# Optimization experiments

Measured on AMD Instinct MI355X. Metric: run time of the kernel, lower is better.

## Reference

```python
import jax, jax.numpy as jnp
import numpy as np


def conv2d(x, w, pad, groups=1):
    # x: [B,Cin,H,W], w: [Cout,Cin/groups,K,K]
    return jax.lax.conv_general_dilated(
        x, w, (1, 1), [(pad, pad), (pad, pad)],
        dimension_numbers=('NCHW', 'OIHW', 'NCHW'),
        feature_group_count=groups)


def setup_inputs() -> dict:
    key = jax.random.key(0)
    ks = jax.random.split(key, 24)
    B, C, H, W = 16, 512, 32, 128          # batch, encoder_dim, feature map
    Da, Ds, De, Dm = 512, 256, 256, 1024   # att_dim, state_dim, embed_dim, mem_dim
    V, Dmerge = 1000, 512
    K, P = 11, 5
    Din = De + C + Dm                       # GRU input dim = 1792
    s = 0.02
    rn = lambda k, shp, sc=1.0: jax.random.normal(k, shp, jnp.float32) * sc
    return {
        'encode': rn(ks[0], (B, C, H, W)),
        'encode_pro': rn(ks[1], (B, Da, H, W)),
        'encode_mask': jnp.ones((B, 1, H, W), jnp.float32),
        'state': rn(ks[2], (B, Ds)),
        'pre_weight': jax.random.uniform(ks[3], (B, 1, H, W), jnp.float32),
        'cum_weight': jax.random.uniform(ks[4], (B, 1, H, W), jnp.float32),
        'context': rn(ks[5], (B, C)),
        'cond_mem': rn(ks[6], (B, Dm)),
        'cond_weight': jax.random.uniform(ks[7], (B, 2, H, W), jnp.float32),
        'label_id': jax.random.randint(ks[8], (B,), 0, V),
        # ImageAttention params (all bias-free per source)
        'w_wt': rn(ks[9], (Da, 1, K, K), s),
        'w_cwt': rn(ks[10], (Da, 1, K, K), s),
        'w_condwt': rn(ks[11], (2 * Da, 1, K, K), s),   # groups=2
        'w_energy': rn(ks[12], (Da,), s),               # 1x1 conv -> vector
        'w_state': rn(ks[13], (Da, Ds), s),
        'w_ctx': rn(ks[14], (Da, C), s),
        'w_cond': rn(ks[15], (Da, Dm), s),
        # GRU params
        'w_i2s': rn(ks[16], (Ds, Din), s), 'b_i2s': jnp.zeros((Ds,), jnp.float32),
        'w_i2g': rn(ks[17], (2 * Ds, Din), s), 'b_i2g': jnp.zeros((2 * Ds,), jnp.float32),
        'w_s2g': rn(ks[18], (2 * Ds, Ds), s),
        'w_h2h': rn(ks[19], (Ds, Ds), s),
        # Readout params
        'embed_table': rn(ks[20], (V, De), s),
        'w_l1': rn(ks[21], (Dmerge, De + Ds + C), s), 'b_l1': jnp.zeros((Dmerge,), jnp.float32),
        'w_l2': rn(ks[22], (V, Dmerge), s), 'b_l2': jnp.zeros((V,), jnp.float32),
    }


def reference(encode, encode_pro, encode_mask, state, pre_weight, cum_weight,
              context, cond_mem, cond_weight, label_id, w_wt, w_cwt, w_condwt,
              w_energy, w_state, w_ctx, w_cond, w_i2s, b_i2s, w_i2g, b_i2g,
              w_s2g, w_h2h, embed_table, w_l1, b_l1, w_l2, b_l2):
    P = (w_wt.shape[-1] - 1) // 2
    Da = w_energy.shape[0]
    B, C, H, W = encode.shape
    # --- ImageAttention ---
    t_pre = conv2d(pre_weight, w_wt, P)           # [B,Da,H,W]
    t_cum = conv2d(cum_weight, w_cwt, P)          # [B,Da,H,W]
    t_cw = conv2d(cond_weight, w_condwt, P, groups=2)
    t_cw = t_cw.reshape(B, 2, Da, H, W).sum(1)    # [B,Da,H,W]
    st = state @ w_state.T + context @ w_ctx.T + cond_mem @ w_cond.T  # [B,Da]
    concat_info = jnp.tanh(st[:, :, None, None] + t_pre + t_cum + t_cw + encode_pro)
    energies = jnp.einsum('bchw,c->bhw', concat_info, w_energy)
    energies = energies + (encode_mask[:, 0] - 1.0) * 1e8
    att = jax.nn.softmax(energies.reshape(B, H * W), axis=1)
    new_weight = att.reshape(B, 1, H, W)
    new_cum_weight = cum_weight + new_weight
    ctx = jnp.einsum('bchw,bhw->bc', encode, new_weight[:, 0])  # [B,C]
    # --- GRU transition (data = [embed, ctx, cond_mem]) ---
    embed = embed_table[label_id]
    data = jnp.concatenate([embed, ctx, cond_mem], axis=1)
    gate = data @ w_i2g.T + b_i2g + state @ w_s2g.T
    Ds = state.shape[1]
    update_g = jax.nn.sigmoid(gate[:, :Ds])
    reset_g = jax.nn.sigmoid(gate[:, Ds:])
    state_hat = jnp.tanh(data @ w_i2s.T + b_i2s + (state * reset_g) @ w_h2h.T)
    new_state = update_g * state_hat + (1.0 - update_g) * state
    # --- Readout.step ---
    merged = jnp.concatenate([embed, new_state, ctx], axis=1)
    hid = jax.nn.relu(merged @ w_l1.T + b_l1)
    readout = hid @ w_l2.T + b_l2                  # [B,V]
    return readout
```

## Files before the change

### kernel.cpp

```cpp
#include <hip/hip_runtime.h>
#include <math.h>

typedef unsigned short u16;
typedef __bf16 bf16x8 __attribute__((ext_vector_type(8)));
typedef float f32x4 __attribute__((ext_vector_type(4)));

__device__ u16   g_A_pack[16 * 512 * 32];
__device__ float g_st[16 * 512];
__device__ float g_epart[2 * 16 * 4096];
__device__ float g_energ[16 * 4096];
__device__ float g_data[16 * 1792];
__device__ float g_merged[16 * 1024];
__device__ float g_update[16 * 256];
__device__ float g_reset[16 * 256];
__device__ float g_i2s[16 * 256];
__device__ float g_hid[16 * 512];

__device__ __forceinline__ u16 f2bf(float f) {
    unsigned u = __float_as_uint(f);
    u = (u + 0x7FFFu + ((u >> 16) & 1u)) >> 16;
    return (u16)u;
}
__device__ __forceinline__ float fast_tanh(float x) {
    return 1.0f - 2.0f / (__expf(2.0f * x) + 1.0f);
}
__device__ __forceinline__ float sigmoidf_(float x) {
    return 1.0f / (1.0f + __expf(-x));
}

__global__ void k_prep(const float* __restrict__ w_wt, const float* __restrict__ w_cwt,
                       const float* __restrict__ w_condwt) {
    int idx = blockIdx.x * blockDim.x + threadIdx.x;
    if (idx >= 512 * 512) return;
    int d = idx >> 9, k = idx & 511;
    float f = 0.f;
    if (k < 484) {
        int c = k / 121, rem = k % 121;
        if (c == 0)      f = w_wt[d * 121 + rem];
        else if (c == 1) f = w_cwt[d * 121 + rem];
        else if (c == 2) f = w_condwt[d * 121 + rem];
        else             f = w_condwt[(512 + d) * 121 + rem];
    }
    int ks = k >> 5, kl = k & 31;
    g_A_pack[(ks * 512 + d) * 32 + kl] = f2bf(f);
}

__global__ void k_st(const float* __restrict__ state, const float* __restrict__ context,
                     const float* __restrict__ cond_mem, const float* __restrict__ w_state,
                     const float* __restrict__ w_ctx, const float* __restrict__ w_cond) {
    int wid = (blockIdx.x * blockDim.x + threadIdx.x) >> 6;
    int lane = threadIdx.x & 63;
    if (wid >= 16 * 512) return;
    int b = wid >> 9, d = wid & 511;
    float acc = 0.f;
    for (int k = lane; k < 256; k += 64)  acc += state[b * 256 + k]    * w_state[d * 256 + k];
    for (int k = lane; k < 512; k += 64)  acc += context[b * 512 + k]  * w_ctx[d * 512 + k];
    for (int k = lane; k < 1024; k += 64) acc += cond_mem[b * 1024 + k] * w_cond[d * 1024 + k];
    for (int off = 32; off; off >>= 1) acc += __shfl_down(acc, off, 64);
    if (lane == 0) g_st[b * 512 + d] = acc;
}

__global__ void k_e0(const int* __restrict__ label, const float* __restrict__ embed_table,
                     const float* __restrict__ cond_mem) {
    int b = blockIdx.x, tid = threadIdx.x;
    int lbl = label[b];
    if (tid < 256) {
        float ev = embed_table[lbl * 256 + tid];
        g_data[b * 1792 + tid] = ev;
        g_merged[b * 1024 + tid] = ev;
    }
    for (int k = tid; k < 1024; k += 256)
        g_data[b * 1792 + 768 + k] = cond_mem[b * 1024 + k];
}

__global__ __launch_bounds__(256, 3) void k_conv_energy(
    const float* __restrict__ pre_w, const float* __restrict__ cum_w, const float* __restrict__ cond_w,
    const float* __restrict__ encode_pro, const float* __restrict__ w_energy)
{
    __shared__ __align__(16) u16 src[4][11][80];
    __shared__ __align__(16) u16 bchunk[2][64][40];
    __shared__ float ered[4][64];

    const int blk = blockIdx.x;
    const int quad = blk & 3;
    const int h = (blk >> 2) & 31;
    const int b = blk >> 7;
    const int dbase = (quad >> 1) * 256;
    const int px0 = (quad & 1) * 64;

    const int tid = threadIdx.x;
    const int lane = tid & 63, wv = tid >> 6;
    const int lr = lane & 15, lg = lane >> 4;

    for (int t = tid; t < 4 * 11 * 80; t += 256) {
        int c = t / (11 * 80);
        int rem = t % (11 * 80);
        int i = rem / 80, x = rem % 80;
        int row = h + i - 5, w = px0 - 5 + x;
        u16 v = 0;
        if (x < 74 && row >= 0 && row < 32 && w >= 0 && w < 128) {
            const float* img = (c == 0) ? pre_w + b * 4096
                             : (c == 1) ? cum_w + b * 4096
                             : (c == 2) ? cond_w + b * 8192
                                        : cond_w + b * 8192 + 4096;
            v = f2bf(img[row * 128 + w]);
        }
        src[c][i][x] = v;
    }
    __syncthreads();

    const int kl = tid & 31;
    const int n0 = tid >> 5;
#define BUILD(KS, BUF)                                                        \
    {                                                                         \
        int kg = (KS) * 32 + kl;                                              \
        int c = 0, i = 0, jj = 0;                                             \
        bool ok = (kg < 484);                                                 \
        if (ok) { c = kg / 121; int r2 = kg % 121; i = r2 / 11; jj = r2 % 11; } \
        _Pragma("unroll")                                                     \
        for (int rep = 0; rep < 8; ++rep) {                                   \
            int n = n0 + rep * 8;                                             \
            bchunk[BUF][n][kl] = ok ? src[c][i][n + jj] : (u16)0;             \
        }                                                                     \
    }

    f32x4 acc[4][4];
#pragma unroll
    for (int mt = 0; mt < 4; ++mt)
#pragma unroll
        for (int nt = 0; nt < 4; ++nt) {
            f32x4 z = {0.f, 0.f, 0.f, 0.f};
            acc[mt][nt] = z;
        }

    BUILD(0, 0);
    __syncthreads();

    for (int ks = 0; ks < 16; ++ks) {
        const int cur = ks & 1;
        bf16x8 afr[4];
#pragma unroll
        for (int mt = 0; mt < 4; ++mt) {
            int d = dbase + wv * 64 + mt * 16 + lr;
            afr[mt] = *reinterpret_cast<const bf16x8*>(&g_A_pack[(ks * 512 + d) * 32 + lg * 8]);
        }
        bf16x8 bfr[4];
#pragma unroll
        for (int nt = 0; nt < 4; ++nt)
            bfr[nt] = *reinterpret_cast<const bf16x8*>(&bchunk[cur][nt * 16 + lr][lg * 8]);

        if (ks < 15) BUILD(ks + 1, cur ^ 1);

#pragma unroll
        for (int mt = 0; mt < 4; ++mt)
#pragma unroll
            for (int nt = 0; nt < 4; ++nt)
                acc[mt][nt] = __builtin_amdgcn_mfma_f32_16x16x32_bf16(afr[mt], bfr[nt], acc[mt][nt], 0, 0, 0);
        __syncthreads();
    }
#undef BUILD

    float e[4] = {0.f, 0.f, 0.f, 0.f};
#pragma unroll
    for (int mt = 0; mt < 4; ++mt) {
#pragma unroll
        for (int r = 0; r < 4; ++r) {
            int d = dbase + wv * 64 + mt * 16 + lg * 4 + r;
            float stv = g_st[b * 512 + d];
            float wev = w_energy[d];
            const float* ep_row = encode_pro + ((size_t)(b * 512 + d) * 32 + h) * 128 + px0;
#pragma unroll
            for (int nt = 0; nt < 4; ++nt) {
                float val = stv + acc[mt][nt][r] + ep_row[nt * 16 + lr];
                e[nt] += wev * fast_tanh(val);
            }
        }
    }
#pragma unroll
    for (int nt = 0; nt < 4; ++nt) {
        float v = e[nt];
        v += __shfl_xor(v, 16, 64);
        v += __shfl_xor(v, 32, 64);
        if (lane < 16) ered[wv][nt * 16 + lane] = v;
    }
    __syncthreads();
    if (tid < 64) {
        float v = ered[0][tid] + ered[1][tid] + ered[2][tid] + ered[3][tid];
        g_epart[(size_t)(quad >> 1) * 65536 + b * 4096 + h * 128 + px0 + tid] = v;
    }
}

__global__ void k_softmax(const float* __restrict__ encode_mask) {
    __shared__ float red[256];
    int b = blockIdx.x, tid = threadIdx.x;
    float v[16];
    float mx = -1e30f;
#pragma unroll
    for (int i = 0; i < 16; ++i) {
        int idx = b * 4096 + tid + i * 256;
        float ev = g_epart[idx] + g_epart[65536 + idx] + (encode_mask[idx] - 1.0f) * 1e8f;
        v[i] = ev; mx = fmaxf(mx, ev);
    }
    red[tid] = mx; __syncthreads();
    for (int s = 128; s; s >>= 1) { if (tid < s) red[tid] = fmaxf(red[tid], red[tid + s]); __syncthreads(); }
    mx = red[0]; __syncthreads();
    float sum = 0.f;
#pragma unroll
    for (int i = 0; i < 16; ++i) { v[i] = __expf(v[i] - mx); sum += v[i]; }
    red[tid] = sum; __syncthreads();
    for (int s = 128; s; s >>= 1) { if (tid < s) red[tid] += red[tid + s]; __syncthreads(); }
    float inv = 1.0f / red[0];
#pragma unroll
    for (int i = 0; i < 16; ++i) g_energ[b * 4096 + tid + i * 256] = v[i] * inv;
}

__global__ void k_ctx(const float* __restrict__ encode) {
    int wid = (blockIdx.x * blockDim.x + threadIdx.x) >> 6;
    int lane = threadIdx.x & 63;
    if (wid >= 16 * 512) return;
    int b = wid >> 9, c = wid & 511;
    const float* e = encode + (size_t)wid * 4096;
    const float* a = g_energ + b * 4096;
    float acc = 0.f;
#pragma unroll
    for (int it = 0; it < 16; ++it) {
        int base = it * 256 + lane * 4;
        float4 ev = *reinterpret_cast<const float4*>(&e[base]);
        float4 av = *reinterpret_cast<const float4*>(&a[base]);
        acc += ev.x * av.x + ev.y * av.y + ev.z * av.z + ev.w * av.w;
    }
    for (int off = 32; off; off >>= 1) acc += __shfl_down(acc, off, 64);
    if (lane == 0) { g_data[b * 1792 + 256 + c] = acc; g_merged[b * 1024 + 512 + c] = acc; }
}

__global__ void k_e1(const float* __restrict__ state,
                     const float* __restrict__ w_i2g, const float* __restrict__ b_i2g,
                     const float* __restrict__ w_s2g, const float* __restrict__ w_i2s,
                     const float* __restrict__ b_i2s) {
    int wid = (blockIdx.x * blockDim.x + threadIdx.x) >> 6;
    int lane = threadIdx.x & 63;
    if (wid >= 16 * 768) return;
    int b = wid / 768, o = wid % 768;
    const float* dt = g_data + b * 1792;
    float acc = 0.f;
    if (o < 512) {
        const float* wr = w_i2g + o * 1792;
        for (int k = lane; k < 1792; k += 64) acc += dt[k] * wr[k];
        const float* wsg = w_s2g + o * 256;
        for (int k = lane; k < 256; k += 64) acc += state[b * 256 + k] * wsg[k];
    } else {
        const float* wr = w_i2s + (o - 512) * 1792;
        for (int k = lane; k < 1792; k += 64) acc += dt[k] * wr[k];
    }
    for (int off = 32; off; off >>= 1) acc += __shfl_down(acc, off, 64);
    if (lane == 0) {
        if (o < 256)       g_update[b * 256 + o]        = sigmoidf_(acc + b_i2g[o]);
        else if (o < 512)  g_reset[b * 256 + (o - 256)] = sigmoidf_(acc + b_i2g[o]);
        else               g_i2s[b * 256 + (o - 512)]   = acc + b_i2s[o - 512];
    }
}

__global__ void k_e2(const float* __restrict__ state, const float* __restrict__ w_h2h) {
    int wid = (blockIdx.x * blockDim.x + threadIdx.x) >> 6;
    int lane = threadIdx.x & 63;
    if (wid >= 16 * 256) return;
    int b = wid >> 8, d = wid & 255;
    const float* wr = w_h2h + d * 256;
    float acc = 0.f;
    for (int k = lane; k < 256; k += 64)
        acc += state[b * 256 + k] * g_reset[b * 256 + k] * wr[k];
    for (int off = 32; off; off >>= 1) acc += __shfl_down(acc, off, 64);
    if (lane == 0) {
        float sh = fast_tanh(g_i2s[b * 256 + d] + acc);
        float u = g_update[b * 256 + d];
        g_merged[b * 1024 + 256 + d] = u * sh + (1.f - u) * state[b * 256 + d];
    }
}

__global__ void k_e3(const float* __restrict__ w_l1, const float* __restrict__ b_l1) {
    int wid = (blockIdx.x * blockDim.x + threadIdx.x) >> 6;
    int lane = threadIdx.x & 63;
    if (wid >= 16 * 512) return;
    int b = wid >> 9, m = wid & 511;
    const float* mg = g_merged + b * 1024;
    const float* wr = w_l1 + m * 1024;
    float acc = 0.f;
    for (int k = lane; k < 1024; k += 64) acc += mg[k] * wr[k];
    for (int off = 32; off; off >>= 1) acc += __shfl_down(acc, off, 64);
    if (lane == 0) g_hid[b * 512 + m] = fmaxf(acc + b_l1[m], 0.f);
}

__global__ void k_e4(const float* __restrict__ w_l2, const float* __restrict__ b_l2,
                     float* __restrict__ out) {
    int wid = (blockIdx.x * blockDim.x + threadIdx.x) >> 6;
    int lane = threadIdx.x & 63;
    if (wid >= 16 * 1000) return;
    int b = wid / 1000, v = wid % 1000;
    const float* hd = g_hid + b * 512;
    const float* wr = w_l2 + v * 512;
    float acc = 0.f;
    for (int k = lane; k < 512; k += 64) acc += hd[k] * wr[k];
    for (int off = 32; off; off >>= 1) acc += __shfl_down(acc, off, 64);
    if (lane == 0) out[b * 1000 + v] = acc + b_l2[v];
}

extern "C" void kernel_launch(void* const* d_in, const int* in_sizes, int n_in,
                              void* d_out, int out_size, void* d_ws, size_t ws_size,
                              hipStream_t stream) {
    static const int EXP[28] = {
        33554432, 33554432, 65536, 4096, 65536, 65536, 8192, 16384, 131072, 16,
        61952, 61952, 123904, 512, 131072, 262144, 524288, 458752, 256, 917504,
        512, 131072, 65536, 256000, 524288, 512, 512000, 1000};
    if (n_in != 28) return;
    for (int i = 0; i < 28; ++i)
        if (in_sizes[i] != EXP[i]) return;

    const float* encode      = (const float*)d_in[0];
    const float* encode_pro  = (const float*)d_in[1];
    const float* encode_mask = (const float*)d_in[2];
    const float* state       = (const float*)d_in[3];
    const float* pre_weight  = (const float*)d_in[4];
    const float* cum_weight  = (const float*)d_in[5];
    const float* context     = (const float*)d_in[6];
    const float* cond_mem    = (const float*)d_in[7];
    const float* cond_weight = (const float*)d_in[8];
    const int*   label_id    = (const int*)d_in[9];
    const float* w_wt     = (const float*)d_in[10];
    const float* w_cwt    = (const float*)d_in[11];
    const float* w_condwt = (const float*)d_in[12];
    const float* w_energy = (const float*)d_in[13];
    const float* w_state  = (const float*)d_in[14];
    const float* w_ctx    = (const float*)d_in[15];
    const float* w_cond   = (const float*)d_in[16];
    const float* w_i2s    = (const float*)d_in[17];
    const float* b_i2s    = (const float*)d_in[18];
    const float* w_i2g    = (const float*)d_in[19];
    const float* b_i2g    = (const float*)d_in[20];
    const float* w_s2g    = (const float*)d_in[21];
    const float* w_h2h    = (const float*)d_in[22];
    const float* embed_t  = (const float*)d_in[23];
    const float* w_l1     = (const float*)d_in[24];
    const float* b_l1     = (const float*)d_in[25];
    const float* w_l2     = (const float*)d_in[26];
    const float* b_l2     = (const float*)d_in[27];
    float* out = (float*)d_out;
    (void)d_ws; (void)ws_size;

    k_prep<<<1024, 256, 0, stream>>>(w_wt, w_cwt, w_condwt);
    k_st<<<2048, 256, 0, stream>>>(state, context, cond_mem, w_state, w_ctx, w_cond);
    k_e0<<<16, 256, 0, stream>>>(label_id, embed_t, cond_mem);
    k_conv_energy<<<2048, 256, 0, stream>>>(pre_weight, cum_weight, cond_weight,
                                            encode_pro, w_energy);
    k_softmax<<<16, 256, 0, stream>>>(encode_mask);
    k_ctx<<<2048, 256, 0, stream>>>(encode);
    k_e1<<<3072, 256, 0, stream>>>(state, w_i2g, b_i2g, w_s2g, w_i2s, b_i2s);
    k_e2<<<1024, 256, 0, stream>>>(state, w_h2h);
    k_e3<<<2048, 256, 0, stream>>>(w_l1, b_l1);
    k_e4<<<4000, 256, 0, stream>>>(w_l2, b_l2, out);
}
```

Before: 188.4 us.

## Build full im2col tile once per block and cover all channels per block

The conv-energy kernel now uses 512-thread blocks that each cover all 512 attention channels for a 64-pixel half-row, instead of splitting channels across two blocks. The im2col B tile for every K chunk is built once into a 64x520 shared buffer before the MFMA loop. This removes the per-step rebuild and barrier, halves the duplicated source staging and im2col work, and drops the two-partial energy sum in softmax. In exchange it uses more shared memory per block, leaves threads beyond 484 filling zero padding, and may lower occupancy.

```diff
diff --git a/kernel.cpp b/kernel.cpp
--- a/kernel.cpp
+++ b/kernel.cpp
@@ -7,7 +7,7 @@
 
 __device__ u16   g_A_pack[16 * 512 * 32];
 __device__ float g_st[16 * 512];
-__device__ float g_epart[2 * 16 * 4096];
+__device__ float g_eraw[16 * 4096];
 __device__ float g_energ[16 * 4096];
 __device__ float g_data[16 * 1792];
 __device__ float g_merged[16 * 1024];
@@ -73,26 +73,25 @@
         g_data[b * 1792 + 768 + k] = cond_mem[b * 1024 + k];
 }
 
-__global__ __launch_bounds__(256, 3) void k_conv_energy(
+__global__ __launch_bounds__(512, 2) void k_conv_energy(
     const float* __restrict__ pre_w, const float* __restrict__ cum_w, const float* __restrict__ cond_w,
     const float* __restrict__ encode_pro, const float* __restrict__ w_energy)
 {
     __shared__ __align__(16) u16 src[4][11][80];
-    __shared__ __align__(16) u16 bchunk[2][64][40];
-    __shared__ float ered[4][64];
+    __shared__ __align__(16) u16 bchunk[64][520];
+    __shared__ float ered[8][64];
 
     const int blk = blockIdx.x;
-    const int quad = blk & 3;
-    const int h = (blk >> 2) & 31;
-    const int b = blk >> 7;
-    const int dbase = (quad >> 1) * 256;
-    const int px0 = (quad & 1) * 64;
+    const int pxh = blk & 1;
+    const int h = (blk >> 1) & 31;
+    const int b = blk >> 6;
+    const int px0 = pxh * 64;
 
     const int tid = threadIdx.x;
     const int lane = tid & 63, wv = tid >> 6;
     const int lr = lane & 15, lg = lane >> 4;
 
-    for (int t = tid; t < 4 * 11 * 80; t += 256) {
+    for (int t = tid; t < 4 * 11 * 80; t += 512) {
         int c = t / (11 * 80);
         int rem = t % (11 * 80);
         int i = rem / 80, x = rem % 80;
@@ -109,20 +108,20 @@
     }
     __syncthreads();
 
-    const int kl = tid & 31;
-    const int n0 = tid >> 5;
-#define BUILD(KS, BUF)                                                        \
-    {                                                                         \
-        int kg = (KS) * 32 + kl;                                              \
-        int c = 0, i = 0, jj = 0;                                             \
-        bool ok = (kg < 484);                                                 \
-        if (ok) { c = kg / 121; int r2 = kg % 121; i = r2 / 11; jj = r2 % 11; } \
-        _Pragma("unroll")                                                     \
-        for (int rep = 0; rep < 8; ++rep) {                                   \
-            int n = n0 + rep * 8;                                             \
-            bchunk[BUF][n][kl] = ok ? src[c][i][n + jj] : (u16)0;             \
-        }                                                                     \
-    }
+    {
+        const int k = tid;
+        if (k < 484) {
+            int c = k / 121, rem = k % 121;
+            int i = rem / 11, jj = rem % 11;
+            const u16* s = &src[c][i][jj];
+#pragma unroll 8
+            for (int n = 0; n < 64; ++n) bchunk[n][k] = s[n];
+        } else {
+#pragma unroll 8
+            for (int n = 0; n < 64; ++n) bchunk[n][k] = 0;
+        }
+    }
+    __syncthreads();
 
     f32x4 acc[4][4];
 #pragma unroll
@@ -133,39 +132,32 @@
             acc[mt][nt] = z;
         }
 
-    BUILD(0, 0);
-    __syncthreads();
-
+#pragma unroll 2
     for (int ks = 0; ks < 16; ++ks) {
-        const int cur = ks & 1;
         bf16x8 afr[4];
 #pragma unroll
         for (int mt = 0; mt < 4; ++mt) {
-            int d = dbase + wv * 64 + mt * 16 + lr;
+            int d = wv * 64 + mt * 16 + lr;
             afr[mt] = *reinterpret_cast<const bf16x8*>(&g_A_pack[(ks * 512 + d) * 32 + lg * 8]);
         }
         bf16x8 bfr[4];
 #pragma unroll
         for (int nt = 0; nt < 4; ++nt)
-            bfr[nt] = *reinterpret_cast<const bf16x8*>(&bchunk[cur][nt * 16 + lr][lg * 8]);
-
-        if (ks < 15) BUILD(ks + 1, cur ^ 1);
+            bfr[nt] = *reinterpret_cast<const bf16x8*>(&bchunk[nt * 16 + lr][ks * 32 + lg * 8]);
 
 #pragma unroll
         for (int mt = 0; mt < 4; ++mt)
 #pragma unroll
             for (int nt = 0; nt < 4; ++nt)
                 acc[mt][nt] = __builtin_amdgcn_mfma_f32_16x16x32_bf16(afr[mt], bfr[nt], acc[mt][nt], 0, 0, 0);
-        __syncthreads();
-    }
-#undef BUILD
+    }
 
     float e[4] = {0.f, 0.f, 0.f, 0.f};
 #pragma unroll
     for (int mt = 0; mt < 4; ++mt) {
 #pragma unroll
         for (int r = 0; r < 4; ++r) {
-            int d = dbase + wv * 64 + mt * 16 + lg * 4 + r;
+            int d = wv * 64 + mt * 16 + lg * 4 + r;
             float stv = g_st[b * 512 + d];
             float wev = w_energy[d];
             const float* ep_row = encode_pro + ((size_t)(b * 512 + d) * 32 + h) * 128 + px0;
@@ -185,8 +177,10 @@
     }
     __syncthreads();
     if (tid < 64) {
-        float v = ered[0][tid] + ered[1][tid] + ered[2][tid] + ered[3][tid];
-        g_epart[(size_t)(quad >> 1) * 65536 + b * 4096 + h * 128 + px0 + tid] = v;
+        float v = 0.f;
+#pragma unroll
+        for (int w = 0; w < 8; ++w) v += ered[w][tid];
+        g_eraw[b * 4096 + h * 128 + px0 + tid] = v;
     }
 }
 
@@ -198,7 +192,7 @@
 #pragma unroll
     for (int i = 0; i < 16; ++i) {
         int idx = b * 4096 + tid + i * 256;
-        float ev = g_epart[idx] + g_epart[65536 + idx] + (encode_mask[idx] - 1.0f) * 1e8f;
+        float ev = g_eraw[idx] + (encode_mask[idx] - 1.0f) * 1e8f;
         v[i] = ev; mx = fmaxf(mx, ev);
     }
     red[tid] = mx; __syncthreads();
@@ -349,7 +343,7 @@
     k_prep<<<1024, 256, 0, stream>>>(w_wt, w_cwt, w_condwt);
     k_st<<<2048, 256, 0, stream>>>(state, context, cond_mem, w_state, w_ctx, w_cond);
     k_e0<<<16, 256, 0, stream>>>(label_id, embed_t, cond_mem);
-    k_conv_energy<<<2048, 256, 0, stream>>>(pre_weight, cum_weight, cond_weight,
+    k_conv_energy<<<1024, 512, 0, stream>>>(pre_weight, cum_weight, cond_weight,
                                             encode_pro, w_energy);
     k_softmax<<<16, 256, 0, stream>>>(encode_mask);
     k_ctx<<<2048, 256, 0, stream>>>(encode);
```

Measured after the change: 194.5 us. 1.03x slower.
